# Performance work log

Measured on AMD Instinct MI355X. Metric: run time of the kernel, lower is better.

Reference implementation:

```python
import jax, jax.numpy as jnp
import numpy as np

B, IN_DIM, OUT_DIM = 4096, 4096, 4096

def setup_inputs() -> dict:
    key = jax.random.key(0)
    kx, kw, kb = jax.random.split(key, 3)
    x = jax.random.normal(kx, (B, IN_DIM), dtype=jnp.float32)
    W = jax.random.normal(kw, (OUT_DIM, IN_DIM), dtype=jnp.float32) * (1.0 / np.sqrt(IN_DIM))
    b = jax.random.normal(kb, (OUT_DIM,), dtype=jnp.float32) * (1.0 / np.sqrt(IN_DIM))
    return {"x": x, "W": W, "b": b}

def reference(x, W, b):
    # Original computes sum over in_dim of x[:, :, None] * W.T[None, :, :],
    # which is exactly x @ W.T. NOTE: bias is added TWICE in the source
    # (duplicated `out += self.b`), so the faithful output is x @ W.T + 2*b.
    out = jnp.einsum('bi,oi->bo', x, W)  # [B, out_dim]
    out = out + 2.0 * b
    return out
```

## Files before the change

kernel.cpp:

```cpp
#include <hip/hip_runtime.h>
#include <hip/hip_bf16.h>
#include <utility>


typedef short bf16x8 __attribute__((ext_vector_type(8)));
typedef short s16x4  __attribute__((ext_vector_type(4)));
typedef short s16x8  __attribute__((ext_vector_type(8)));
typedef float f32x4  __attribute__((ext_vector_type(4)));

constexpr int MDIM = 4096, NDIM = 4096, KDIM = 4096;

typedef const __attribute__((address_space(1))) void* gas_t;
typedef __attribute__((address_space(3))) void*       las_t;

__device__ __forceinline__ short f2bf(float f) {
    __hip_bfloat16 h = __float2bfloat16(f);
    short s; __builtin_memcpy(&s, &h, 2); return s;
}

__global__ __launch_bounds__(256)
void cvt2_f32_bf16(const float* __restrict__ inA, const float* __restrict__ inB,
                   short* __restrict__ outA, short* __restrict__ outB, int n8each) {
    int idx    = blockIdx.x * blockDim.x + threadIdx.x;
    int stride = gridDim.x * blockDim.x;
    for (int i = idx; i < 2 * n8each; i += stride) {
        const f32x4* in4 = (i < n8each) ? (const f32x4*)inA : (const f32x4*)inB;
        s16x8*      out8 = (i < n8each) ? (s16x8*)outA      : (s16x8*)outB;
        int j = (i < n8each) ? i : i - n8each;
        f32x4 a = in4[2 * j];
        f32x4 b = in4[2 * j + 1];
        s16x8 o = { f2bf(a[0]), f2bf(a[1]), f2bf(a[2]), f2bf(a[3]),
                    f2bf(b[0]), f2bf(b[1]), f2bf(b[2]), f2bf(b[3]) };
        out8[j] = o;
    }
}

constexpr int BM = 256, BN = 256, BK = 64;
constexpr int NT  = KDIM / BK;
constexpr int ASZ = BM * BK;
constexpr int BSZ = BN * BK;

template <int Q>
__device__ __forceinline__ void read_aq(const short* base, int rA, int c0, int c1,
                                        bf16x8 (&dst)[2][2]) {
    #pragma unroll
    for (int m = 0; m < 2; ++m) {
        const short* p = &base[(rA + Q * 32 + m * 16) * BK];
        dst[m][0] = *(const bf16x8*)(p + c0);
        dst[m][1] = *(const bf16x8*)(p + c1);
    }
}

template <int Q>
__device__ __forceinline__ void mfma_quad(const bf16x8 (&af)[2][2], const bf16x8 (&bf)[4][2],
                                          f32x4 (&acc)[8][4]) {
    __builtin_amdgcn_s_setprio(1);
    #pragma unroll
    for (int m = 0; m < 2; ++m)
        #pragma unroll
        for (int ni = 0; ni < 4; ++ni)
            #pragma unroll
            for (int kk = 0; kk < 2; ++kk)
                acc[Q * 2 + m][ni] = __builtin_amdgcn_mfma_f32_16x16x32_bf16(
                    af[m][kk], bf[ni][kk], acc[Q * 2 + m][ni], 0, 0, 0);
    __builtin_amdgcn_s_setprio(0);
}

__global__ __launch_bounds__(512, 2)
void gemm_bf16_256(const short* __restrict__ Xb, const short* __restrict__ Wb,
                   const float* __restrict__ Bv, float* __restrict__ Out)
{
    __shared__ short lds[2 * ASZ + 2 * BSZ];

    const int tid  = threadIdx.x;
    const int lane = tid & 63;
    const int wid  = tid >> 6;
    const int wr   = wid >> 2;
    const int wc   = wid & 3;

    const int bid = blockIdx.x;
    const int lin = (bid & 7) * 32 + (bid >> 3);
    const int tm0 = (lin >> 4) * BM;
    const int tn0 = (lin & 15) * BN;

    const int srow = lane >> 3;
    const int sgrn = (lane & 7) ^ srow;
    const char* xbase = (const char*)Xb;
    const char* wbase = (const char*)Wb;
    int aOff[2][2], bOff[2][2], dOff[2][2];
    #pragma unroll
    for (int h = 0; h < 2; ++h) {
        #pragma unroll
        for (int j = 0; j < 2; ++j) {
            const int r = h * 128 + (2 * wid + j) * 8;
            aOff[h][j] = ((tm0 + r + srow) * KDIM + sgrn * 8) * 2;
            bOff[h][j] = ((tn0 + r + srow) * KDIM + sgrn * 8) * 2;
            dOff[h][j] = r * BK;
        }
    }

    const int g   = lane >> 4;
    const int r16 = lane & 15;
    const int c0  = ((0 + g) ^ (r16 & 7)) * 8;
    const int c1  = ((4 + g) ^ (r16 & 7)) * 8;
    const int rA  = wr * 128 + r16;
    const int rB  = wc * 64  + r16;

    f32x4 acc[8][4] = {};
    bf16x8 bf[4][2];
    bf16x8 a0[2][2];

    auto tile_body = [&](auto par_ic, int t) {
        constexpr int PAR = decltype(par_ic)::value;
        const short* Ab  = (const short*)&lds[PAR * ASZ];
        const short* AbN = (const short*)&lds[(PAR ^ 1) * ASZ];
        const short* BbN = (const short*)&lds[2 * ASZ + (PAR ^ 1) * BSZ];
        short* dstA = (short*)&lds[(PAR ^ 1) * ASZ];
        short* dstB = (short*)&lds[2 * ASZ + PAR * BSZ];

        auto stageA = [&](int kt, int h) {
            const size_t kb = (size_t)kt * (BK * 2);
            __builtin_amdgcn_global_load_lds((gas_t)(xbase + kb + aOff[h][0]),
                                             (las_t)(dstA + dOff[h][0]), 16, 0, 0);
            __builtin_amdgcn_global_load_lds((gas_t)(xbase + kb + aOff[h][1]),
                                             (las_t)(dstA + dOff[h][1]), 16, 0, 0);
        };
        auto stageB = [&](int kt, int h) {
            const size_t kb = (size_t)kt * (BK * 2);
            __builtin_amdgcn_global_load_lds((gas_t)(wbase + kb + bOff[h][0]),
                                             (las_t)(dstB + dOff[h][0]), 16, 0, 0);
            __builtin_amdgcn_global_load_lds((gas_t)(wbase + kb + bOff[h][1]),
                                             (las_t)(dstB + dOff[h][1]), 16, 0, 0);
        };

        bf16x8 aq1[2][2];
        read_aq<1>(Ab, rA, c0, c1, aq1);
        if (t + 1 < NT) { stageA(t + 1, 0); stageA(t + 1, 1); }
        mfma_quad<0>(a0, bf, acc);

        bf16x8 aq2[2][2];
        read_aq<2>(Ab, rA, c0, c1, aq2);
        if (t + 2 < NT) stageB(t + 2, 0);
        mfma_quad<1>(aq1, bf, acc);

        bf16x8 aq3[2][2];
        read_aq<3>(Ab, rA, c0, c1, aq3);
        if (t + 2 < NT) stageB(t + 2, 1);
        if (t < NT - 2) { asm volatile("s_waitcnt vmcnt(4)" ::: "memory"); }
        else            { asm volatile("s_waitcnt vmcnt(0)" ::: "memory"); }
        asm volatile("s_barrier" ::: "memory");
        mfma_quad<2>(aq2, bf, acc);

        mfma_quad<3>(aq3, bf, acc);
        if (t + 1 < NT) {
            #pragma unroll
            for (int ni = 0; ni < 4; ++ni) {
                const short* p = &BbN[(rB + ni * 16) * BK];
                bf[ni][0] = *(const bf16x8*)(p + c0);
                bf[ni][1] = *(const bf16x8*)(p + c1);
            }
            read_aq<0>(AbN, rA, c0, c1, a0);
        }
        asm volatile("s_barrier" ::: "memory");
    };

    {
        short* dA0 = (short*)&lds[0];
        short* dB0 = (short*)&lds[2 * ASZ];
        short* dB1 = (short*)&lds[2 * ASZ + BSZ];
        #pragma unroll
        for (int h = 0; h < 2; ++h) {
            __builtin_amdgcn_global_load_lds((gas_t)(wbase + bOff[h][0]), (las_t)(dB0 + dOff[h][0]), 16, 0, 0);
            __builtin_amdgcn_global_load_lds((gas_t)(wbase + bOff[h][1]), (las_t)(dB0 + dOff[h][1]), 16, 0, 0);
        }
        #pragma unroll
        for (int h = 0; h < 2; ++h) {
            __builtin_amdgcn_global_load_lds((gas_t)(xbase + aOff[h][0]), (las_t)(dA0 + dOff[h][0]), 16, 0, 0);
            __builtin_amdgcn_global_load_lds((gas_t)(xbase + aOff[h][1]), (las_t)(dA0 + dOff[h][1]), 16, 0, 0);
        }
        #pragma unroll
        for (int h = 0; h < 2; ++h) {
            __builtin_amdgcn_global_load_lds((gas_t)(wbase + (BK * 2) + bOff[h][0]), (las_t)(dB1 + dOff[h][0]), 16, 0, 0);
            __builtin_amdgcn_global_load_lds((gas_t)(wbase + (BK * 2) + bOff[h][1]), (las_t)(dB1 + dOff[h][1]), 16, 0, 0);
        }
        asm volatile("s_waitcnt vmcnt(4)" ::: "memory");
        asm volatile("s_barrier" ::: "memory");
        const short* Bb0 = (const short*)&lds[2 * ASZ];
        #pragma unroll
        for (int ni = 0; ni < 4; ++ni) {
            const short* p = &Bb0[(rB + ni * 16) * BK];
            bf[ni][0] = *(const bf16x8*)(p + c0);
            bf[ni][1] = *(const bf16x8*)(p + c1);
        }
        read_aq<0>((const short*)&lds[0], rA, c0, c1, a0);
    }

    for (int t = 0; t < NT; t += 2) {
        tile_body(std::integral_constant<int, 0>{}, t);
        tile_body(std::integral_constant<int, 1>{}, t + 1);
    }

    float bb[4];
    #pragma unroll
    for (int ni = 0; ni < 4; ++ni)
        bb[ni] = 2.0f * Bv[tn0 + wc * 64 + ni * 16 + r16];

    #pragma unroll
    for (int mi = 0; mi < 8; ++mi) {
        #pragma unroll
        for (int r = 0; r < 4; ++r) {
            const int row = tm0 + wr * 128 + mi * 16 + g * 4 + r;
            float* orow = Out + (size_t)row * NDIM + tn0 + wc * 64 + r16;
            #pragma unroll
            for (int ni = 0; ni < 4; ++ni)
                orow[ni * 16] = acc[mi][ni][r] + bb[ni];
        }
    }
}

constexpr int FBM = 128, FBN = 128, FBK = 32, LDT = FBK + 8;
__global__ __launch_bounds__(256)
void gemm_xwt_bias2(const float* __restrict__ X, const float* __restrict__ W,
                    const float* __restrict__ Bv, float* __restrict__ Out)
{
    __shared__ short As[FBM * LDT];
    __shared__ short Bs[FBN * LDT];
    const int tid  = threadIdx.x;
    const int lane = tid & 63;
    const int wid  = tid >> 6;
    const int wr   = wid >> 1;
    const int wc   = wid & 1;
    const int tm0  = blockIdx.y * FBM;
    const int tn0  = blockIdx.x * FBN;
    const int srow = tid >> 3;
    const int scol = (tid & 7) * 4;
    const int g    = lane >> 4;
    const int r16  = lane & 15;
    f32x4 acc[4][4] = {};
    const float* xg = X + (size_t)(tm0 + srow) * KDIM + scol;
    const float* wg = W + (size_t)(tn0 + srow) * KDIM + scol;
    for (int k0 = 0; k0 < KDIM; k0 += FBK) {
        #pragma unroll
        for (int i = 0; i < 4; ++i) {
            const int row = srow + 32 * i;
            f32x4 av = *(const f32x4*)(xg + (size_t)(32 * i) * KDIM + k0);
            f32x4 bv = *(const f32x4*)(wg + (size_t)(32 * i) * KDIM + k0);
            s16x4 pa = { f2bf(av[0]), f2bf(av[1]), f2bf(av[2]), f2bf(av[3]) };
            s16x4 pb = { f2bf(bv[0]), f2bf(bv[1]), f2bf(bv[2]), f2bf(bv[3]) };
            *(s16x4*)&As[row * LDT + scol] = pa;
            *(s16x4*)&Bs[row * LDT + scol] = pb;
        }
        __syncthreads();
        bf16x8 af[4], bfr[4];
        #pragma unroll
        for (int mi = 0; mi < 4; ++mi)
            af[mi] = *(const bf16x8*)&As[(wr * 64 + mi * 16 + r16) * LDT + g * 8];
        #pragma unroll
        for (int ni = 0; ni < 4; ++ni)
            bfr[ni] = *(const bf16x8*)&Bs[(wc * 64 + ni * 16 + r16) * LDT + g * 8];
        #pragma unroll
        for (int mi = 0; mi < 4; ++mi)
            #pragma unroll
            for (int ni = 0; ni < 4; ++ni)
                acc[mi][ni] = __builtin_amdgcn_mfma_f32_16x16x32_bf16(
                                  af[mi], bfr[ni], acc[mi][ni], 0, 0, 0);
        __syncthreads();
    }
    float bb[4];
    #pragma unroll
    for (int ni = 0; ni < 4; ++ni)
        bb[ni] = 2.0f * Bv[tn0 + wc * 64 + ni * 16 + r16];
    #pragma unroll
    for (int mi = 0; mi < 4; ++mi)
        #pragma unroll
        for (int r = 0; r < 4; ++r) {
            const int row = tm0 + wr * 64 + mi * 16 + g * 4 + r;
            float* orow = Out + (size_t)row * NDIM + tn0 + wc * 64 + r16;
            #pragma unroll
            for (int ni = 0; ni < 4; ++ni)
                orow[ni * 16] = acc[mi][ni][r] + bb[ni];
        }
}

extern "C" void kernel_launch(void* const* d_in, const int* in_sizes, int n_in,
                              void* d_out, int out_size, void* d_ws, size_t ws_size,
                              hipStream_t stream) {
    const float* X  = (const float*)d_in[0];
    const float* W  = (const float*)d_in[1];
    const float* Bv = (const float*)d_in[2];
    float* Out = (float*)d_out;

    const size_t nElem = (size_t)MDIM * KDIM;
    const size_t need  = 2 * nElem * sizeof(short);

    if (ws_size >= need) {
        short* Xb = (short*)d_ws;
        short* Wb = Xb + nElem;
        const int n8 = (int)(nElem / 8);
        cvt2_f32_bf16<<<4096, 256, 0, stream>>>(X, W, Xb, Wb, n8);
        gemm_bf16_256<<<dim3(256), 512, 0, stream>>>(Xb, Wb, Bv, Out);
    } else {
        dim3 grid(NDIM / FBN, MDIM / FBM);
        gemm_xwt_bias2<<<grid, 256, 0, stream>>>(X, W, Bv, Out);
    }
}
```

Before: 140.5 us.

## Split A-tile prefetch across iterations and reorder MFMA loop by k

The first half of the next A tile is now issued a full iteration earlier, into the buffer just consumed after the mid-tile barrier, while the second half stays at the start of the tile. This spreads the global-to-LDS loads more evenly through the iteration, and the prologue adds one extra A half-load. The MFMA inner loop is also reordered to iterate over k first, changing how dependent accumulator updates are spaced. It risks overwriting LDS rows that other waves are still reading if the barrier placement is wrong, and the vmcnt accounting must stay consistent.

```diff
diff --git a/kernel.cpp b/kernel.cpp
--- a/kernel.cpp
+++ b/kernel.cpp
@@ -56,11 +56,11 @@
                                           f32x4 (&acc)[8][4]) {
     __builtin_amdgcn_s_setprio(1);
     #pragma unroll
-    for (int m = 0; m < 2; ++m)
-        #pragma unroll
-        for (int ni = 0; ni < 4; ++ni)
-            #pragma unroll
-            for (int kk = 0; kk < 2; ++kk)
+    for (int kk = 0; kk < 2; ++kk)
+        #pragma unroll
+        for (int m = 0; m < 2; ++m)
+            #pragma unroll
+            for (int ni = 0; ni < 4; ++ni)
                 acc[Q * 2 + m][ni] = __builtin_amdgcn_mfma_f32_16x16x32_bf16(
                     af[m][kk], bf[ni][kk], acc[Q * 2 + m][ni], 0, 0, 0);
     __builtin_amdgcn_s_setprio(0);
@@ -110,47 +110,49 @@
     bf16x8 bf[4][2];
     bf16x8 a0[2][2];
 
+    auto stageAh = [&](int kt, int h, short* dst) {
+        const size_t kb = (size_t)kt * (BK * 2);
+        __builtin_amdgcn_global_load_lds((gas_t)(xbase + kb + aOff[h][0]),
+                                         (las_t)(dst + dOff[h][0]), 16, 0, 0);
+        __builtin_amdgcn_global_load_lds((gas_t)(xbase + kb + aOff[h][1]),
+                                         (las_t)(dst + dOff[h][1]), 16, 0, 0);
+    };
+    auto stageBh = [&](int kt, int h, short* dst) {
+        const size_t kb = (size_t)kt * (BK * 2);
+        __builtin_amdgcn_global_load_lds((gas_t)(wbase + kb + bOff[h][0]),
+                                         (las_t)(dst + dOff[h][0]), 16, 0, 0);
+        __builtin_amdgcn_global_load_lds((gas_t)(wbase + kb + bOff[h][1]),
+                                         (las_t)(dst + dOff[h][1]), 16, 0, 0);
+    };
+
     auto tile_body = [&](auto par_ic, int t) {
         constexpr int PAR = decltype(par_ic)::value;
         const short* Ab  = (const short*)&lds[PAR * ASZ];
         const short* AbN = (const short*)&lds[(PAR ^ 1) * ASZ];
         const short* BbN = (const short*)&lds[2 * ASZ + (PAR ^ 1) * BSZ];
-        short* dstA = (short*)&lds[(PAR ^ 1) * ASZ];
-        short* dstB = (short*)&lds[2 * ASZ + PAR * BSZ];
-
-        auto stageA = [&](int kt, int h) {
-            const size_t kb = (size_t)kt * (BK * 2);
-            __builtin_amdgcn_global_load_lds((gas_t)(xbase + kb + aOff[h][0]),
-                                             (las_t)(dstA + dOff[h][0]), 16, 0, 0);
-            __builtin_amdgcn_global_load_lds((gas_t)(xbase + kb + aOff[h][1]),
-                                             (las_t)(dstA + dOff[h][1]), 16, 0, 0);
-        };
-        auto stageB = [&](int kt, int h) {
-            const size_t kb = (size_t)kt * (BK * 2);
-            __builtin_amdgcn_global_load_lds((gas_t)(wbase + kb + bOff[h][0]),
-                                             (las_t)(dstB + dOff[h][0]), 16, 0, 0);
-            __builtin_amdgcn_global_load_lds((gas_t)(wbase + kb + bOff[h][1]),
-                                             (las_t)(dstB + dOff[h][1]), 16, 0, 0);
-        };
+        short* dstA1 = (short*)&lds[(PAR ^ 1) * ASZ];
+        short* dstA2 = (short*)&lds[PAR * ASZ];
+        short* dstB  = (short*)&lds[2 * ASZ + PAR * BSZ];
 
         bf16x8 aq1[2][2];
         read_aq<1>(Ab, rA, c0, c1, aq1);
-        if (t + 1 < NT) { stageA(t + 1, 0); stageA(t + 1, 1); }
+        if (t + 1 < NT) stageAh(t + 1, 1, dstA1);
         mfma_quad<0>(a0, bf, acc);
 
         bf16x8 aq2[2][2];
         read_aq<2>(Ab, rA, c0, c1, aq2);
-        if (t + 2 < NT) stageB(t + 2, 0);
+        if (t + 2 < NT) stageBh(t + 2, 0, dstB);
         mfma_quad<1>(aq1, bf, acc);
 
         bf16x8 aq3[2][2];
         read_aq<3>(Ab, rA, c0, c1, aq3);
-        if (t + 2 < NT) stageB(t + 2, 1);
+        if (t + 2 < NT) stageBh(t + 2, 1, dstB);
         if (t < NT - 2) { asm volatile("s_waitcnt vmcnt(4)" ::: "memory"); }
         else            { asm volatile("s_waitcnt vmcnt(0)" ::: "memory"); }
         asm volatile("s_barrier" ::: "memory");
         mfma_quad<2>(aq2, bf, acc);
 
+        if (t + 2 < NT) stageAh(t + 2, 0, dstA2);
         mfma_quad<3>(aq3, bf, acc);
         if (t + 1 < NT) {
             #pragma unroll
@@ -166,24 +168,17 @@
 
     {
         short* dA0 = (short*)&lds[0];
+        short* dA1 = (short*)&lds[ASZ];
         short* dB0 = (short*)&lds[2 * ASZ];
         short* dB1 = (short*)&lds[2 * ASZ + BSZ];
         #pragma unroll
-        for (int h = 0; h < 2; ++h) {
-            __builtin_amdgcn_global_load_lds((gas_t)(wbase + bOff[h][0]), (las_t)(dB0 + dOff[h][0]), 16, 0, 0);
-            __builtin_amdgcn_global_load_lds((gas_t)(wbase + bOff[h][1]), (las_t)(dB0 + dOff[h][1]), 16, 0, 0);
-        }
-        #pragma unroll
-        for (int h = 0; h < 2; ++h) {
-            __builtin_amdgcn_global_load_lds((gas_t)(xbase + aOff[h][0]), (las_t)(dA0 + dOff[h][0]), 16, 0, 0);
-            __builtin_amdgcn_global_load_lds((gas_t)(xbase + aOff[h][1]), (las_t)(dA0 + dOff[h][1]), 16, 0, 0);
-        }
-        #pragma unroll
-        for (int h = 0; h < 2; ++h) {
-            __builtin_amdgcn_global_load_lds((gas_t)(wbase + (BK * 2) + bOff[h][0]), (las_t)(dB1 + dOff[h][0]), 16, 0, 0);
-            __builtin_amdgcn_global_load_lds((gas_t)(wbase + (BK * 2) + bOff[h][1]), (las_t)(dB1 + dOff[h][1]), 16, 0, 0);
-        }
-        asm volatile("s_waitcnt vmcnt(4)" ::: "memory");
+        for (int h = 0; h < 2; ++h) stageBh(0, h, dB0);
+        #pragma unroll
+        for (int h = 0; h < 2; ++h) stageAh(0, h, dA0);
+        #pragma unroll
+        for (int h = 0; h < 2; ++h) stageBh(1, h, dB1);
+        stageAh(1, 0, dA1);
+        asm volatile("s_waitcnt vmcnt(6)" ::: "memory");
         asm volatile("s_barrier" ::: "memory");
         const short* Bb0 = (const short*)&lds[2 * ASZ];
         #pragma unroll
```

Measured after the change: 151.1 us. 7.5% more time.
